# Performance work log

Hardware: AMD Instinct MI355X
Metric: run time of the kernel (lower is better)

Reference implementation:

```python
import jax, jax.numpy as jnp
import numpy as np

B, S, D = 2, 2048, 1024
N_QK, N_V, N_KNOW = 4096, 4096, 8192
N_HEADS = 16
MAX_K_QK, MAX_K_V, MAX_K_KNOW = 32, 32, 64
LN_EPS = 1e-6


def _unit_norm(key, shape, scale=1.0):
    x = jax.random.normal(key, shape, jnp.float32)
    return x / (jnp.linalg.norm(x, axis=-1, keepdims=True) + 1e-8) * scale


def setup_inputs() -> dict:
    key = jax.random.key(0)
    ks = jax.random.split(key, 12)
    return {
        "x": jax.random.normal(ks[0], (B, S, D), jnp.float32),
        "qk_emb": _unit_norm(ks[1], (N_QK, D)),
        "qk_w": _unit_norm(ks[2], (N_QK, D)),
        "v_emb": _unit_norm(ks[3], (N_V, D)),
        "v_w": _unit_norm(ks[4], (N_V, D)),
        "know_emb": _unit_norm(ks[5], (N_KNOW, D)),
        "know_w": _unit_norm(ks[6], (N_KNOW, D)),
        "tau_attn_k": jax.random.normal(ks[7], (D, 3), jnp.float32) * (1.0 / np.sqrt(D)),
        "tau_attn_b": jnp.zeros((3,), jnp.float32),
        "tau_know_k": jax.random.normal(ks[8], (D, 1), jnp.float32) * (1.0 / np.sqrt(D)),
        "tau_know_b": jnp.zeros((1,), jnp.float32),
        "expand_O": jax.random.normal(ks[9], (D, D), jnp.float32) * 0.02,
        "ln1_scale": jnp.ones((D,), jnp.float32),
        "ln1_bias": jnp.zeros((D,), jnp.float32),
        "ln2_scale": jnp.ones((D,), jnp.float32),
        "ln2_bias": jnp.zeros((D,), jnp.float32),
    }


def _layer_norm(x, scale, bias):
    mean = jnp.mean(x, axis=-1, keepdims=True)
    var = jnp.mean(jnp.square(x - mean), axis=-1, keepdims=True)
    return (x - mean) / jnp.sqrt(var + LN_EPS) * scale + bias


def threshold_gate(scores, tau, max_k):
    # scores: [B,S,N], tau: [B,S,1]
    raw = scores - tau
    gate = jnp.where(raw > 0, raw, 1e-8 * jnp.exp(raw))
    exp_gate = jnp.exp(gate) - 1.0
    topk_vals, _ = jax.lax.top_k(exp_gate, min(max_k, scores.shape[-1]))
    thr = topk_vals[:, :, -1:]
    exp_gate = jnp.where(exp_gate >= thr, exp_gate, 0.0)
    gate_sum = exp_gate.sum(axis=-1, keepdims=True) + 1e-8
    strength = jnp.tanh(exp_gate.max(axis=-1, keepdims=True))
    return exp_gate / gate_sum * strength


@jax.checkpoint
def sense_emit_full(x, emb, w, gate):
    # [B,S,D] @ [D,N] -> gated [B,S,N] -> [B,S,D]
    return ((x @ emb.T) * gate) @ w


def _block(x, qk_emb, qk_w, v_emb, v_w, know_emb, know_w,
           tau_attn_k, tau_attn_b, tau_know_k, tau_know_b,
           expand_O, ln1_scale, ln1_bias, ln2_scale, ln2_bias):
    # ---- attention circuit (deterministic; dropout = identity) ----
    normed = _layer_norm(x, ln1_scale, ln1_bias)
    scores_qk = normed @ qk_emb.T           # [B,S,N_QK]
    scores_v = normed @ v_emb.T             # [B,S,N_V]
    tau_all = normed @ tau_attn_k + tau_attn_b  # [B,S,3]
    g_Q = threshold_gate(scores_qk, tau_all[:, :, 0:1], MAX_K_QK)
    g_K = threshold_gate(scores_qk, tau_all[:, :, 1:2], MAX_K_QK)
    g_V = threshold_gate(scores_v, tau_all[:, :, 2:3], MAX_K_V)
    t_qk = 1.0 / qk_emb.shape[0]
    t_v = 1.0 / v_emb.shape[0]
    a_aux = (((g_Q.mean(axis=(0, 1)) - t_qk) ** 2).sum() * g_Q.shape[-1]
             + ((g_K.mean(axis=(0, 1)) - t_qk) ** 2).sum() * g_K.shape[-1]
             + ((g_V.mean(axis=(0, 1)) - t_v) ** 2).sum() * g_V.shape[-1])

    Q = sense_emit_full(normed, qk_emb, qk_w, g_Q)
    K = sense_emit_full(normed, qk_emb, qk_w, g_K)
    V = sense_emit_full(normed, v_emb, v_w, g_V)

    Bs, Ss, Ds = x.shape
    d_head = Ds // N_HEADS
    Q = Q.reshape(Bs, Ss, N_HEADS, d_head).transpose(0, 2, 1, 3)
    K = K.reshape(Bs, Ss, N_HEADS, d_head).transpose(0, 2, 1, 3)
    V = V.reshape(Bs, Ss, N_HEADS, d_head).transpose(0, 2, 1, 3)
    scale = jnp.sqrt(jnp.float32(d_head))
    attn = jnp.einsum('bhsd,bhtd->bhst', Q, K) / scale
    causal = jnp.tril(jnp.ones((Ss, Ss), dtype=jnp.bool_))
    attn = jnp.where(causal, attn, jnp.finfo(attn.dtype).min)
    attn = jax.nn.softmax(attn, axis=-1)
    out = jnp.einsum('bhst,bhtd->bhsd', attn, V)
    out = out.transpose(0, 2, 1, 3).reshape(Bs, Ss, Ds)
    out = out @ expand_O
    x = x + out

    # ---- knowledge circuit ----
    normed = _layer_norm(x, ln2_scale, ln2_bias)
    scores_k = normed @ know_emb.T          # [B,S,N_KNOW]
    tau_k = normed @ tau_know_k + tau_know_b
    gate = threshold_gate(scores_k, tau_k, MAX_K_KNOW)
    t_k = 1.0 / know_emb.shape[0]
    k_aux = ((gate.mean(axis=(0, 1)) - t_k) ** 2).sum() * know_emb.shape[0]
    know_out = sense_emit_full(normed, know_emb, know_w, gate)
    x = x + know_out
    return x, a_aux + k_aux


def reference(x, qk_emb, qk_w, v_emb, v_w, know_emb, know_w,
              tau_attn_k, tau_attn_b, tau_know_k, tau_know_b,
              expand_O, ln1_scale, ln1_bias, ln2_scale, ln2_bias):
    return _block(x, qk_emb, qk_w, v_emb, v_w, know_emb, know_w,
                  tau_attn_k, tau_attn_b, tau_know_k, tau_know_b,
                  expand_O, ln1_scale, ln1_bias, ln2_scale, ln2_bias)
```

## Files before the change

kernel.cpp:

```cpp
#include <hip/hip_runtime.h>

#define TOK   4096
#define DIM   1024
#define NQK   4096
#define NV    4096
#define NKN   8192
#define SLEN  2048
#define NH    16
#define DH    64
#define CAPA  48
#define CAPK  96
#define APAD  72

typedef float  f32x4  __attribute__((ext_vector_type(4)));
typedef short  short8 __attribute__((ext_vector_type(8)));
typedef unsigned int  u32;
typedef unsigned short u16;

__device__ __forceinline__ u16 f2bf(float f) {
    u32 u = __float_as_uint(f);
    u32 r = (u + 0x7fffu + ((u >> 16) & 1u)) >> 16;
    return (u16)r;
}
__device__ __forceinline__ float bf2f(u16 v) { return __uint_as_float(((u32)v) << 16); }

__device__ __forceinline__ u16 bfkey(u16 b) {
    return (b & 0x8000u) ? (u16)(~b) : (u16)(b | 0x8000u);
}
__device__ __forceinline__ u16 keybf(u16 k) {
    return (k & 0x8000u) ? (u16)(k & 0x7fffu) : (u16)(~k);
}

__device__ __forceinline__ f32x4 mfma_bf16(short8 a, short8 b, f32x4 c) {
    asm volatile("v_mfma_f32_16x16x32_bf16 %0, %1, %2, %0"
                 : "+v"(c) : "v"(a), "v"(b));
    return c;
}

__device__ __forceinline__ void gload16(const u16* g, u16* s) {
    __builtin_amdgcn_global_load_lds((const __attribute__((address_space(1))) void*)g,
                                     (__attribute__((address_space(3))) void*)s, 16, 0, 0);
}

__device__ __forceinline__ float blockReduceF(float v, float* red, int wave, int lane) {
#pragma unroll
    for (int off = 32; off > 0; off >>= 1) v += __shfl_xor(v, off);
    __syncthreads();
    if (lane == 0) red[wave] = v;
    __syncthreads();
    return red[0] + red[1] + red[2] + red[3];
}

__global__ __launch_bounds__(256) void k_convert_all(const float* __restrict__ p0,
                                                     const float* __restrict__ p1,
                                                     const float* __restrict__ p2,
                                                     const float* __restrict__ p3,
                                                     const float* __restrict__ p4,
                                                     const float* __restrict__ p5,
                                                     u16* __restrict__ o0, u16* __restrict__ o1,
                                                     u16* __restrict__ o2, u16* __restrict__ o3,
                                                     u16* __restrict__ o4, u16* __restrict__ o5) {
    const int S0 = 1048576, S1 = 2097152, S2 = 4194304, S3 = 5242880, S4 = 6291456, S5 = 8388608;
    for (int i = blockIdx.x * 256 + threadIdx.x; i < S5; i += gridDim.x * 256) {
        const float* in; u16* out; int off;
        if (i < S0)      { in = p0; out = o0; off = i; }
        else if (i < S1) { in = p1; out = o1; off = i - S0; }
        else if (i < S2) { in = p2; out = o2; off = i - S1; }
        else if (i < S3) { in = p3; out = o3; off = i - S2; }
        else if (i < S4) { in = p4; out = o4; off = i - S3; }
        else             { in = p5; out = o5; off = i - S4; }
        float4 v = reinterpret_cast<const float4*>(in)[off];
        reinterpret_cast<ushort4*>(out)[off] = make_ushort4(f2bf(v.x), f2bf(v.y), f2bf(v.z), f2bf(v.w));
    }
}

__global__ __launch_bounds__(256) void k_transpose_bf16(const float* __restrict__ in,
                                                        u16* __restrict__ out) {
    __shared__ float tile[32][33];
    int bx = blockIdx.x * 32;
    int by = blockIdx.y * 32;
    int tx = threadIdx.x & 31;
    int ty = threadIdx.x >> 5;
    for (int r = ty; r < 32; r += 8)
        tile[r][tx] = in[(size_t)(by + r) * DIM + bx + tx];
    __syncthreads();
    for (int r = ty; r < 32; r += 8)
        out[(size_t)(bx + r) * DIM + by + tx] = f2bf(tile[tx][r]);
}

__global__ __launch_bounds__(256) void k_ln_tau(const float* __restrict__ x,
                                                const float* __restrict__ sc,
                                                const float* __restrict__ bi,
                                                const float* __restrict__ tauk,
                                                const float* __restrict__ taub,
                                                int ntau,
                                                u16* __restrict__ nrm,
                                                float* __restrict__ tau_out) {
    __shared__ float red[4];
    int t = blockIdx.x, tid = threadIdx.x, wave = tid >> 6, lane = tid & 63;
    const float4 xv = reinterpret_cast<const float4*>(x + (size_t)t * DIM)[tid];
    float s = xv.x + xv.y + xv.z + xv.w;
    s = blockReduceF(s, red, wave, lane);
    float mean = s * (1.0f / DIM);
    float d0 = xv.x - mean, d1 = xv.y - mean, d2 = xv.z - mean, d3 = xv.w - mean;
    float ss = d0 * d0 + d1 * d1 + d2 * d2 + d3 * d3;
    ss = blockReduceF(ss, red, wave, lane);
    float rstd = rsqrtf(ss * (1.0f / DIM) + 1e-6f);
    const float4 scv = reinterpret_cast<const float4*>(sc)[tid];
    const float4 biv = reinterpret_cast<const float4*>(bi)[tid];
    float n0 = d0 * rstd * scv.x + biv.x;
    float n1 = d1 * rstd * scv.y + biv.y;
    float n2 = d2 * rstd * scv.z + biv.z;
    float n3 = d3 * rstd * scv.w + biv.w;
    ushort4 o = make_ushort4(f2bf(n0), f2bf(n1), f2bf(n2), f2bf(n3));
    reinterpret_cast<ushort4*>(nrm + (size_t)t * DIM)[tid] = o;
    int d = tid * 4;
    for (int j = 0; j < ntau; j++) {
        float p = n0 * tauk[(size_t)(d + 0) * ntau + j] + n1 * tauk[(size_t)(d + 1) * ntau + j]
                + n2 * tauk[(size_t)(d + 2) * ntau + j] + n3 * tauk[(size_t)(d + 3) * ntau + j];
        p = blockReduceF(p, red, wave, lane);
        if (tid == 0) tau_out[(size_t)t * ntau + j] = p + taub[j];
    }
}

template<int TAG, int KEYOUT>
__global__ __launch_bounds__(256) void k_gemm_bt(const u16* __restrict__ A,
                                                 const u16* __restrict__ B,
                                                 void* __restrict__ Cv,
                                                 int M, int N, int K,
                                                 const float* __restrict__ res) {
    __shared__ __align__(16) u16 As[4096];
    __shared__ __align__(16) u16 Bs[4096];
    int tid = threadIdx.x;
    int wave = tid >> 6, lane = tid & 63;
    int m0 = blockIdx.y * 128, n0 = blockIdx.x * 128;
    int wm = (wave >> 1) * 64, wn = (wave & 1) * 64;
    int kg = lane >> 4, l15 = lane & 15;

    const u16* gA0 = A + (size_t)(m0 + lane) * K + wave * 8;
    const u16* gA1 = A + (size_t)(m0 + 64 + lane) * K + wave * 8;
    const u16* gB0 = B + (size_t)(n0 + lane) * K + wave * 8;
    const u16* gB1 = B + (size_t)(n0 + 64 + lane) * K + wave * 8;
    u16* sA0 = As + wave * 1024;
    u16* sA1 = As + wave * 1024 + 512;
    u16* sB0 = Bs + wave * 1024;
    u16* sB1 = Bs + wave * 1024 + 512;

    f32x4 acc[4][4];
#pragma unroll
    for (int i = 0; i < 4; i++)
#pragma unroll
        for (int j = 0; j < 4; j++) { f32x4 z = {0.f, 0.f, 0.f, 0.f}; acc[i][j] = z; }

    for (int k0 = 0; k0 < K; k0 += 32) {
        __syncthreads();
        gload16(gA0 + k0, sA0);
        gload16(gA1 + k0, sA1);
        gload16(gB0 + k0, sB0);
        gload16(gB1 + k0, sB1);
        __syncthreads();
        short8 af[4], bg[4];
#pragma unroll
        for (int mi = 0; mi < 4; mi++) {
            int row = wm + mi * 16 + l15;
            af[mi] = *reinterpret_cast<const short8*>(&As[(kg * 128 + row) * 8]);
        }
#pragma unroll
        for (int ni = 0; ni < 4; ni++) {
            int row = wn + ni * 16 + l15;
            bg[ni] = *reinterpret_cast<const short8*>(&Bs[(kg * 128 + row) * 8]);
        }
#pragma unroll
        for (int mi = 0; mi < 4; mi++)
#pragma unroll
            for (int ni = 0; ni < 4; ni++)
                acc[mi][ni] = mfma_bf16(af[mi], bg[ni], acc[mi][ni]);
    }
    asm volatile("s_nop 7\n\ts_nop 7");
#pragma unroll
    for (int mi = 0; mi < 4; mi++) {
#pragma unroll
        for (int ni = 0; ni < 4; ni++) {
            int col = n0 + wn + ni * 16 + l15;
#pragma unroll
            for (int r = 0; r < 4; r++) {
                int rowm = m0 + wm + mi * 16 + (lane >> 4) * 4 + r;
                size_t idx = (size_t)rowm * N + col;
                float v = acc[mi][ni][r];
                if (KEYOUT) {
                    ((u16*)Cv)[idx] = bfkey(f2bf(v));
                } else {
                    if (res) v += res[idx];
                    ((float*)Cv)[idx] = v;
                }
            }
        }
    }
}

__global__ __launch_bounds__(256) void k_gate(const u16* __restrict__ keys_g, int NC, int ksel,
                                              int row_off,
                                              const float* __restrict__ tau, int tau_stride, int tcol0,
                                              int two,
                                              int* __restrict__ sel,
                                              float* __restrict__ vA, float* __restrict__ vB,
                                              int* __restrict__ cnt,
                                              float* __restrict__ csA, float* __restrict__ csB,
                                              int cap) {
    extern __shared__ u16 keys[];
    __shared__ int   hist[256];
    __shared__ int   scnt;
    __shared__ int   dsel;
    __shared__ int   knext;
    __shared__ int   sidx[CAPK];
    __shared__ float sraw[CAPK];
    int r = blockIdx.x, tid = threadIdx.x, wave = tid >> 6, lane = tid & 63;
    int t = row_off + r;

    const uint4* srow8 = reinterpret_cast<const uint4*>(keys_g + (size_t)r * NC);
    for (int c = tid; c < NC / 8; c += 256)
        reinterpret_cast<uint4*>(keys)[c] = srow8[c];
    if (tid == 0) scnt = 0;

    u32 prefix = 0;
    int krem = ksel;
#pragma unroll
    for (int pass = 0; pass < 2; pass++) {
        int shift = 8 - pass * 8;
        hist[tid] = 0;
        __syncthreads();
        u32 pmask = (pass == 0) ? 0u : 0xFF00u;
        for (int i = tid; i < NC; i += 256) {
            u32 ky = keys[i];
            if ((ky & pmask) == prefix)
                atomicAdd(&hist[(ky >> shift) & 255], 1);
        }
        __syncthreads();
        int v = hist[tid];
#pragma unroll
        for (int off = 1; off < 256; off <<= 1) {
            int other = (tid + off < 256) ? hist[tid + off] : 0;
            __syncthreads();
            v += other;
            hist[tid] = v;
            __syncthreads();
        }
        int sfx = v;
        int sfx_next = (tid < 255) ? hist[tid + 1] : 0;
        if (sfx >= krem && (tid == 255 || sfx_next < krem)) {
            dsel = tid;
            knext = krem - sfx_next;
        }
        __syncthreads();
        prefix |= ((u32)dsel) << shift;
        krem = knext;
        __syncthreads();
    }
    u32 thr = prefix;

    for (int i = tid; i < NC; i += 256) {
        u32 ky = keys[i];
        if (ky >= thr) {
            int p = atomicAdd(&scnt, 1);
            if (p < cap) {
                sidx[p] = i;
                sraw[p] = bf2f(keybf((u16)ky));
            }
        }
    }
    __syncthreads();
    int n = scnt < cap ? scnt : cap;
    if (tid == 0) cnt[t] = n;
    if (wave != 0) return;

    float tA = tau[(size_t)t * tau_stride + tcol0];
    float tB = two ? tau[(size_t)t * tau_stride + tcol0 + 1] : 0.f;
    float sumA = 0.f, mxA = -1e30f, sumB = 0.f, mxB = -1e30f;
    for (int i = lane; i < n; i += 64) {
        float sv = sraw[i];
        float rA = sv - tA;
        float gA = rA > 0.f ? rA : 1e-8f * expf(rA);
        float eA = expf(gA) - 1.0f;
        sumA += eA; mxA = fmaxf(mxA, eA);
        if (two) {
            float rB = sv - tB;
            float gB = rB > 0.f ? rB : 1e-8f * expf(rB);
            float eB = expf(gB) - 1.0f;
            sumB += eB; mxB = fmaxf(mxB, eB);
        }
    }
#pragma unroll
    for (int off = 32; off > 0; off >>= 1) {
        sumA += __shfl_xor(sumA, off); mxA = fmaxf(mxA, __shfl_xor(mxA, off));
        sumB += __shfl_xor(sumB, off); mxB = fmaxf(mxB, __shfl_xor(mxB, off));
    }
    float fA = tanhf(mxA) / (sumA + 1e-8f);
    float fB = tanhf(mxB) / (sumB + 1e-8f);
    for (int i = lane; i < n; i += 64) {
        float sv = sraw[i]; int ci = sidx[i];
        float rA = sv - tA;
        float gA = rA > 0.f ? rA : 1e-8f * expf(rA);
        float ga = (expf(gA) - 1.0f) * fA;
        sel[(size_t)t * cap + i] = ci;
        vA[(size_t)t * cap + i] = ga * sv;
        atomicAdd(&csA[ci], ga);
        if (two) {
            float rB = sv - tB;
            float gB = rB > 0.f ? rB : 1e-8f * expf(rB);
            float gb = (expf(gB) - 1.0f) * fB;
            vB[(size_t)t * cap + i] = gb * sv;
            atomicAdd(&csB[ci], gb);
        }
    }
}

__global__ __launch_bounds__(256) void k_gather2(const u16* __restrict__ w,
                                                 const int* __restrict__ sel,
                                                 const float* __restrict__ vA,
                                                 const float* __restrict__ vB,
                                                 const int* __restrict__ cnt, int cap,
                                                 u16* __restrict__ OA, u16* __restrict__ OB) {
    __shared__ int   sI[CAPK];
    __shared__ float sA[CAPK];
    __shared__ float sB[CAPK];
    int t = blockIdx.x, tid = threadIdx.x;
    int n = cnt[t];
    if (tid < n) { sI[tid] = sel[(size_t)t * cap + tid]; sA[tid] = vA[(size_t)t * cap + tid]; sB[tid] = vB[(size_t)t * cap + tid]; }
    __syncthreads();
    float a0 = 0, a1 = 0, a2 = 0, a3 = 0, b0 = 0, b1 = 0, b2 = 0, b3 = 0;
    for (int s = 0; s < n; s++) {
        const ushort4 wv = reinterpret_cast<const ushort4*>(w + (size_t)sI[s] * DIM)[tid];
        float w0 = bf2f(wv.x), w1 = bf2f(wv.y), w2 = bf2f(wv.z), w3 = bf2f(wv.w);
        float va = sA[s], vb = sB[s];
        a0 += va * w0; a1 += va * w1; a2 += va * w2; a3 += va * w3;
        b0 += vb * w0; b1 += vb * w1; b2 += vb * w2; b3 += vb * w3;
    }
    reinterpret_cast<ushort4*>(OA + (size_t)t * DIM)[tid] = make_ushort4(f2bf(a0), f2bf(a1), f2bf(a2), f2bf(a3));
    reinterpret_cast<ushort4*>(OB + (size_t)t * DIM)[tid] = make_ushort4(f2bf(b0), f2bf(b1), f2bf(b2), f2bf(b3));
}

__global__ __launch_bounds__(256) void k_gather1(const u16* __restrict__ w,
                                                 const int* __restrict__ sel,
                                                 const float* __restrict__ vv,
                                                 const int* __restrict__ cnt, int cap,
                                                 u16* __restrict__ O) {
    __shared__ int   sI[CAPK];
    __shared__ float sV[CAPK];
    int t = blockIdx.x, tid = threadIdx.x;
    int n = cnt[t];
    if (tid < n) { sI[tid] = sel[(size_t)t * cap + tid]; sV[tid] = vv[(size_t)t * cap + tid]; }
    __syncthreads();
    float a0 = 0, a1 = 0, a2 = 0, a3 = 0;
    for (int s = 0; s < n; s++) {
        const ushort4 wv = reinterpret_cast<const ushort4*>(w + (size_t)sI[s] * DIM)[tid];
        float va = sV[s];
        a0 += va * bf2f(wv.x); a1 += va * bf2f(wv.y); a2 += va * bf2f(wv.z); a3 += va * bf2f(wv.w);
    }
    reinterpret_cast<ushort4*>(O + (size_t)t * DIM)[tid] = make_ushort4(f2bf(a0), f2bf(a1), f2bf(a2), f2bf(a3));
}

__global__ __launch_bounds__(256) void k_gather_final(const u16* __restrict__ w,
                                                      const int* __restrict__ sel,
                                                      const float* __restrict__ vv,
                                                      const int* __restrict__ cnt, int cap,
                                                      float* __restrict__ io) {
    __shared__ int   sI[CAPK];
    __shared__ float sV[CAPK];
    int t = blockIdx.x, tid = threadIdx.x;
    int n = cnt[t];
    if (tid < n) { sI[tid] = sel[(size_t)t * cap + tid]; sV[tid] = vv[(size_t)t * cap + tid]; }
    __syncthreads();
    float4 base = reinterpret_cast<const float4*>(io + (size_t)t * DIM)[tid];
    float a0 = base.x, a1 = base.y, a2 = base.z, a3 = base.w;
    for (int s = 0; s < n; s++) {
        const ushort4 wv = reinterpret_cast<const ushort4*>(w + (size_t)sI[s] * DIM)[tid];
        float va = sV[s];
        a0 += va * bf2f(wv.x); a1 += va * bf2f(wv.y); a2 += va * bf2f(wv.z); a3 += va * bf2f(wv.w);
    }
    reinterpret_cast<float4*>(io + (size_t)t * DIM)[tid] = make_float4(a0, a1, a2, a3);
}

__global__ __launch_bounds__(256) void k_attn(const u16* __restrict__ Q,
                                              const u16* __restrict__ K,
                                              const u16* __restrict__ V,
                                              u16* __restrict__ O) {
    __shared__ __align__(16) u16 Qs[64 * APAD];
    __shared__ __align__(16) u16 Ks[64 * APAD];
    __shared__ __align__(16) u16 Vt[64 * APAD];
    __shared__ __align__(16) u16 Ps[4][16 * APAD];
    int tid = threadIdx.x, wave = tid >> 6, lane = tid & 63;
    int qt = gridDim.x - 1 - blockIdx.x;
    int h = blockIdx.y, bb = blockIdx.z;
    int q0 = qt * 64;
    size_t base = ((size_t)bb * SLEN) * DIM + (size_t)h * DH;
    int sr = tid >> 2, sc = (tid & 3) * 16;
    int g = lane >> 4, l15 = lane & 15;

    {
        const u16* qp = Q + base + (size_t)(q0 + sr) * DIM + sc;
        *reinterpret_cast<short8*>(&Qs[sr * APAD + sc])     = *reinterpret_cast<const short8*>(qp);
        *reinterpret_cast<short8*>(&Qs[sr * APAD + sc + 8]) = *reinterpret_cast<const short8*>(qp + 8);
    }
    __syncthreads();
    short8 qa0 = *reinterpret_cast<const short8*>(&Qs[(wave * 16 + l15) * APAD + g * 8]);
    short8 qa1 = *reinterpret_cast<const short8*>(&Qs[(wave * 16 + l15) * APAD + 32 + g * 8]);

    float m[4], l[4];
    f32x4 oacc[4];
#pragma unroll
    for (int i = 0; i < 4; i++) {
        m[i] = -1e30f; l[i] = 0.f;
        f32x4 z = {0.f, 0.f, 0.f, 0.f}; oacc[i] = z;
    }
    u16* pw = &Ps[wave][0];

    for (int kc = 0; kc <= qt; kc++) {
        __syncthreads();
        {
            const u16* kp = K + base + (size_t)(kc * 64 + sr) * DIM + sc;
            *reinterpret_cast<short8*>(&Ks[sr * APAD + sc])     = *reinterpret_cast<const short8*>(kp);
            *reinterpret_cast<short8*>(&Ks[sr * APAD + sc + 8]) = *reinterpret_cast<const short8*>(kp + 8);
            const u16* vp = V + base + (size_t)(kc * 64 + sr) * DIM + sc;
            short8 w0 = *reinterpret_cast<const short8*>(vp);
            short8 w1 = *reinterpret_cast<const short8*>(vp + 8);
            const u16* w0p = reinterpret_cast<const u16*>(&w0);
            const u16* w1p = reinterpret_cast<const u16*>(&w1);
#pragma unroll
            for (int j = 0; j < 16; j++) {
                int d = sc + j;
                int phys = (((sr >> 3) + d + (d >> 4)) & 7);
                Vt[d * APAD + phys * 8 + (sr & 7)] = (j < 8) ? w0p[j] : w1p[j - 8];
            }
        }
        __syncthreads();

        f32x4 s4[4];
#pragma unroll
        for (int ks = 0; ks < 4; ks++) {
            f32x4 z = {0.f, 0.f, 0.f, 0.f}; s4[ks] = z;
            short8 kb0 = *reinterpret_cast<const short8*>(&Ks[(ks * 16 + l15) * APAD + g * 8]);
            short8 kb1 = *reinterpret_cast<const short8*>(&Ks[(ks * 16 + l15) * APAD + 32 + g * 8]);
            s4[ks] = mfma_bf16(qa0, kb0, s4[ks]);
            s4[ks] = mfma_bf16(qa1, kb1, s4[ks]);
        }
        asm volatile("s_nop 7\n\ts_nop 7");

        int key_base = kc * 64 + l15;
#pragma unroll
        for (int ks = 0; ks < 4; ks++) {
            int key = key_base + ks * 16;
#pragma unroll
            for (int r = 0; r < 4; r++) {
                int q_abs = q0 + wave * 16 + g * 4 + r;
                float sv = s4[ks][r] * 0.125f;
                s4[ks][r] = (key > q_abs) ? -1e30f : sv;
            }
        }

#pragma unroll
        for (int r = 0; r < 4; r++) {
            float mx = fmaxf(fmaxf(s4[0][r], s4[1][r]), fmaxf(s4[2][r], s4[3][r]));
            mx = fmaxf(mx, __shfl_xor(mx, 1));
            mx = fmaxf(mx, __shfl_xor(mx, 2));
            mx = fmaxf(mx, __shfl_xor(mx, 4));
            mx = fmaxf(mx, __shfl_xor(mx, 8));
            float mnew = fmaxf(m[r], mx);
            float al = __expf(m[r] - mnew);
            m[r] = mnew;
            float p0 = __expf(s4[0][r] - mnew);
            float p1 = __expf(s4[1][r] - mnew);
            float p2 = __expf(s4[2][r] - mnew);
            float p3 = __expf(s4[3][r] - mnew);
            float ps = p0 + p1 + p2 + p3;
            ps += __shfl_xor(ps, 1);
            ps += __shfl_xor(ps, 2);
            ps += __shfl_xor(ps, 4);
            ps += __shfl_xor(ps, 8);
            l[r] = l[r] * al + ps;
#pragma unroll
            for (int ds_ = 0; ds_ < 4; ds_++) oacc[ds_][r] *= al;
            int row = g * 4 + r;
            pw[row * APAD +  0 + l15] = f2bf(p0);
            pw[row * APAD + 16 + l15] = f2bf(p1);
            pw[row * APAD + 32 + l15] = f2bf(p2);
            pw[row * APAD + 48 + l15] = f2bf(p3);
        }

        short8 pa0 = *reinterpret_cast<const short8*>(&pw[l15 * APAD + g * 8]);
        short8 pa1 = *reinterpret_cast<const short8*>(&pw[l15 * APAD + 32 + g * 8]);
#pragma unroll
        for (int dsub = 0; dsub < 4; dsub++) {
            int d = dsub * 16 + l15;
            int rot = d + (d >> 4);
            short8 vb0 = *reinterpret_cast<const short8*>(&Vt[d * APAD + (((0 + g) + rot) & 7) * 8]);
            short8 vb1 = *reinterpret_cast<const short8*>(&Vt[d * APAD + (((4 + g) + rot) & 7) * 8]);
            oacc[dsub] = mfma_bf16(pa0, vb0, oacc[dsub]);
            oacc[dsub] = mfma_bf16(pa1, vb1, oacc[dsub]);
        }
    }
    asm volatile("s_nop 7\n\ts_nop 7");

#pragma unroll
    for (int r = 0; r < 4; r++) {
        float inv = 1.0f / l[r];
        int row = q0 + wave * 16 + g * 4 + r;
#pragma unroll
        for (int dsub = 0; dsub < 4; dsub++) {
            O[base + (size_t)row * DIM + dsub * 16 + l15] = f2bf(oacc[dsub][r] * inv);
        }
    }
}

__global__ __launch_bounds__(256) void k_aux(const float* __restrict__ cs,
                                             float* __restrict__ out_aux) {
    __shared__ float red[4];
    int gtid = blockIdx.x * 256 + threadIdx.x;
    float acc = 0.f;
    for (int i = gtid; i < 3 * 4096 + 8192; i += gridDim.x * 256) {
        float mean = cs[i] * (1.0f / 4096.0f);
        float tN, Nf;
        if (i < 12288) { tN = 1.0f / 4096.0f; Nf = 4096.0f; }
        else           { tN = 1.0f / 8192.0f; Nf = 8192.0f; }
        float d = mean - tN;
        acc += d * d * Nf;
    }
    acc = blockReduceF(acc, red, threadIdx.x >> 6, threadIdx.x & 63);
    if (threadIdx.x == 0) atomicAdd(out_aux, acc);
}

extern "C" void kernel_launch(void* const* d_in, const int* in_sizes, int n_in,
                              void* d_out, int out_size, void* d_ws, size_t ws_size,
                              hipStream_t stream) {
    const float* x         = (const float*)d_in[0];
    const float* qk_emb    = (const float*)d_in[1];
    const float* qk_w      = (const float*)d_in[2];
    const float* v_emb     = (const float*)d_in[3];
    const float* v_w       = (const float*)d_in[4];
    const float* know_emb  = (const float*)d_in[5];
    const float* know_w    = (const float*)d_in[6];
    const float* tau_attn_k = (const float*)d_in[7];
    const float* tau_attn_b = (const float*)d_in[8];
    const float* tau_know_k = (const float*)d_in[9];
    const float* tau_know_b = (const float*)d_in[10];
    const float* expand_O  = (const float*)d_in[11];
    const float* ln1_s     = (const float*)d_in[12];
    const float* ln1_b     = (const float*)d_in[13];
    const float* ln2_s     = (const float*)d_in[14];
    const float* ln2_b     = (const float*)d_in[15];
    float* out = (float*)d_out;
    char*  ws  = (char*)d_ws;

    u16*   nrm_bf   = (u16*)(ws + 0);
    u16*   qkemb_bf = (u16*)(ws + 8388608);
    u16*   vemb_bf  = (u16*)(ws + 16777216);
    u16*   knemb_bf = (u16*)(ws + 25165824);
    u16*   expT_bf  = (u16*)(ws + 41943040);
    u16*   attn_bf  = (u16*)(ws + 44040192);
    u16*   qkw_bf   = (u16*)(ws + 52428800);
    u16*   vw_bf    = (u16*)(ws + 60817408);
    u16*   knw_bf   = (u16*)(ws + 69206016);
    u16*   Qb       = (u16*)(ws + 85983232);
    u16*   Kb       = (u16*)(ws + 94371840);
    u16*   Vb       = (u16*)(ws + 102760448);
    u16*   keysbuf  = (u16*)(ws + 111149056);
    int*   selQK    = (int*)(ws + 178257920);
    float* valQ     = (float*)(ws + 179044352);
    float* valK     = (float*)(ws + 179830784);
    int*   selV     = (int*)(ws + 180617216);
    float* valV     = (float*)(ws + 181403648);
    int*   selKn    = (int*)(ws + 182190080);
    float* valKn    = (float*)(ws + 183762944);
    int*   cntQK    = (int*)(ws + 185335808);
    int*   cntV     = (int*)(ws + 185352192);
    int*   cntKn    = (int*)(ws + 185368576);
    float* tauA     = (float*)(ws + 185384960);
    float* tauKn    = (float*)(ws + 185434112);
    float* colsum   = (float*)(ws + 185450496);
    const size_t WS_NEEDED = 185532416;
    if (ws_size < WS_NEEDED) return;

    float* colQ = colsum, *colK = colsum + 4096, *colV = colsum + 8192, *colKn = colsum + 12288;

    hipMemsetAsync(colsum, 0, 20480 * sizeof(float), stream);
    hipMemsetAsync(out + (size_t)TOK * DIM, 0, sizeof(float), stream);

    k_convert_all<<<2048, 256, 0, stream>>>(qk_emb, v_emb, know_emb, qk_w, v_w, know_w,
                                            qkemb_bf, vemb_bf, knemb_bf, qkw_bf, vw_bf, knw_bf);
    k_transpose_bf16<<<dim3(32, 32), 256, 0, stream>>>(expand_O, expT_bf);

    k_ln_tau<<<TOK, 256, 0, stream>>>(x, ln1_s, ln1_b, tau_attn_k, tau_attn_b, 3, nrm_bf, tauA);

    k_gemm_bt<0, 1><<<dim3(NQK / 128, TOK / 128), 256, 0, stream>>>(nrm_bf, qkemb_bf, keysbuf, TOK, NQK, DIM, nullptr);
    k_gate<<<TOK, 256, NQK * sizeof(u16), stream>>>(keysbuf, NQK, 32, 0, tauA, 3, 0, 1,
                                                    selQK, valQ, valK, cntQK, colQ, colK, CAPA);
    k_gemm_bt<1, 1><<<dim3(NV / 128, TOK / 128), 256, 0, stream>>>(nrm_bf, vemb_bf, keysbuf, TOK, NV, DIM, nullptr);
    k_gate<<<TOK, 256, NV * sizeof(u16), stream>>>(keysbuf, NV, 32, 0, tauA, 3, 2, 0,
                                                   selV, valV, nullptr, cntV, colV, nullptr, CAPA);

    k_gather2<<<TOK, 256, 0, stream>>>(qkw_bf, selQK, valQ, valK, cntQK, CAPA, Qb, Kb);
    k_gather1<<<TOK, 256, 0, stream>>>(vw_bf, selV, valV, cntV, CAPA, Vb);

    k_attn<<<dim3(SLEN / 64, NH, 2), 256, 0, stream>>>(Qb, Kb, Vb, attn_bf);

    k_gemm_bt<2, 0><<<dim3(DIM / 128, TOK / 128), 256, 0, stream>>>(attn_bf, expT_bf, out, TOK, DIM, DIM, x);

    k_ln_tau<<<TOK, 256, 0, stream>>>(out, ln2_s, ln2_b, tau_know_k, tau_know_b, 1, nrm_bf, tauKn);

    for (int c = 0; c < 2; c++) {
        k_gemm_bt<3, 1><<<dim3(NKN / 128, 2048 / 128), 256, 0, stream>>>(
            nrm_bf + (size_t)c * 2048 * DIM, knemb_bf, keysbuf, 2048, NKN, DIM, nullptr);
        k_gate<<<2048, 256, NKN * sizeof(u16), stream>>>(keysbuf, NKN, 64, c * 2048, tauKn, 1, 0, 0,
                                                         selKn, valKn, nullptr, cntKn, colKn, nullptr, CAPK);
    }

    k_gather_final<<<TOK, 256, 0, stream>>>(knw_bf, selKn, valKn, cntKn, CAPK, out);

    k_aux<<<20, 256, 0, stream>>>(colsum, out + (size_t)TOK * DIM);
}
```

Before: 818.6 us.

## Fuse gating with sparse weight gather and reorder attention grid

Merges the threshold-gate kernel with the following sparse gather/emit kernels. Each block selects its top-k indices, computes gate values in shared memory, then immediately accumulates the selected weight rows, with the gather loop unrolled by four. This removes the global sel/val/cnt round trip and three kernel launches. The attention grid is also reordered so heads and batches vary fastest with the query tile outermost, which changes the causal load-balancing order. The cost is that gating now holds the large keys buffer in shared memory through the gather phase, which may lower occupancy.

```diff
diff --git a/kernel.cpp b/kernel.cpp
--- a/kernel.cpp
+++ b/kernel.cpp
@@ -198,24 +198,25 @@
     }
 }
 
-__global__ __launch_bounds__(256) void k_gate(const u16* __restrict__ keys_g, int NC, int ksel,
-                                              int row_off,
-                                              const float* __restrict__ tau, int tau_stride, int tcol0,
-                                              int two,
-                                              int* __restrict__ sel,
-                                              float* __restrict__ vA, float* __restrict__ vB,
-                                              int* __restrict__ cnt,
-                                              float* __restrict__ csA, float* __restrict__ csB,
-                                              int cap) {
+template<int TWO, int RES>
+__global__ __launch_bounds__(256) void k_gate_emit(const u16* __restrict__ keys_g, int NC, int ksel,
+                                                   int row_off,
+                                                   const float* __restrict__ tau, int tau_stride, int tcol0,
+                                                   const u16* __restrict__ w,
+                                                   u16* __restrict__ OA, u16* __restrict__ OB,
+                                                   float* __restrict__ io,
+                                                   float* __restrict__ csA, float* __restrict__ csB) {
     extern __shared__ u16 keys[];
     __shared__ int   hist[256];
     __shared__ int   scnt;
     __shared__ int   dsel;
     __shared__ int   knext;
     __shared__ int   sidx[CAPK];
-    __shared__ float sraw[CAPK];
+    __shared__ float svA[CAPK];
+    __shared__ float svB[CAPK];
     int r = blockIdx.x, tid = threadIdx.x, wave = tid >> 6, lane = tid & 63;
     int t = row_off + r;
+    const int cap = TWO ? CAPA : (RES ? CAPK : CAPA);
 
     const uint4* srow8 = reinterpret_cast<const uint4*>(keys_g + (size_t)r * NC);
     for (int c = tid; c < NC / 8; c += 256)
@@ -264,120 +265,111 @@
             int p = atomicAdd(&scnt, 1);
             if (p < cap) {
                 sidx[p] = i;
-                sraw[p] = bf2f(keybf((u16)ky));
+                svA[p] = bf2f(keybf((u16)ky));
             }
         }
     }
     __syncthreads();
     int n = scnt < cap ? scnt : cap;
-    if (tid == 0) cnt[t] = n;
-    if (wave != 0) return;
-
-    float tA = tau[(size_t)t * tau_stride + tcol0];
-    float tB = two ? tau[(size_t)t * tau_stride + tcol0 + 1] : 0.f;
-    float sumA = 0.f, mxA = -1e30f, sumB = 0.f, mxB = -1e30f;
-    for (int i = lane; i < n; i += 64) {
-        float sv = sraw[i];
-        float rA = sv - tA;
-        float gA = rA > 0.f ? rA : 1e-8f * expf(rA);
-        float eA = expf(gA) - 1.0f;
-        sumA += eA; mxA = fmaxf(mxA, eA);
-        if (two) {
-            float rB = sv - tB;
-            float gB = rB > 0.f ? rB : 1e-8f * expf(rB);
-            float eB = expf(gB) - 1.0f;
-            sumB += eB; mxB = fmaxf(mxB, eB);
-        }
-    }
-#pragma unroll
-    for (int off = 32; off > 0; off >>= 1) {
-        sumA += __shfl_xor(sumA, off); mxA = fmaxf(mxA, __shfl_xor(mxA, off));
-        sumB += __shfl_xor(sumB, off); mxB = fmaxf(mxB, __shfl_xor(mxB, off));
-    }
-    float fA = tanhf(mxA) / (sumA + 1e-8f);
-    float fB = tanhf(mxB) / (sumB + 1e-8f);
-    for (int i = lane; i < n; i += 64) {
-        float sv = sraw[i]; int ci = sidx[i];
-        float rA = sv - tA;
-        float gA = rA > 0.f ? rA : 1e-8f * expf(rA);
-        float ga = (expf(gA) - 1.0f) * fA;
-        sel[(size_t)t * cap + i] = ci;
-        vA[(size_t)t * cap + i] = ga * sv;
-        atomicAdd(&csA[ci], ga);
-        if (two) {
-            float rB = sv - tB;
-            float gB = rB > 0.f ? rB : 1e-8f * expf(rB);
-            float gb = (expf(gB) - 1.0f) * fB;
-            vB[(size_t)t * cap + i] = gb * sv;
-            atomicAdd(&csB[ci], gb);
-        }
-    }
-}
-
-__global__ __launch_bounds__(256) void k_gather2(const u16* __restrict__ w,
-                                                 const int* __restrict__ sel,
-                                                 const float* __restrict__ vA,
-                                                 const float* __restrict__ vB,
-                                                 const int* __restrict__ cnt, int cap,
-                                                 u16* __restrict__ OA, u16* __restrict__ OB) {
-    __shared__ int   sI[CAPK];
-    __shared__ float sA[CAPK];
-    __shared__ float sB[CAPK];
-    int t = blockIdx.x, tid = threadIdx.x;
-    int n = cnt[t];
-    if (tid < n) { sI[tid] = sel[(size_t)t * cap + tid]; sA[tid] = vA[(size_t)t * cap + tid]; sB[tid] = vB[(size_t)t * cap + tid]; }
+
+    if (wave == 0) {
+        float tA = tau[(size_t)t * tau_stride + tcol0];
+        float tB = TWO ? tau[(size_t)t * tau_stride + tcol0 + 1] : 0.f;
+        float sumA = 0.f, mxA = -1e30f, sumB = 0.f, mxB = -1e30f;
+        float sv0 = (lane < n) ? svA[lane] : 0.f;
+        float sv1 = (lane + 64 < n) ? svA[lane + 64] : 0.f;
+        for (int i = lane; i < n; i += 64) {
+            float sv = svA[i];
+            float rA = sv - tA;
+            float gA = rA > 0.f ? rA : 1e-8f * expf(rA);
+            float eA = expf(gA) - 1.0f;
+            sumA += eA; mxA = fmaxf(mxA, eA);
+            if (TWO) {
+                float rB = sv - tB;
+                float gB = rB > 0.f ? rB : 1e-8f * expf(rB);
+                float eB = expf(gB) - 1.0f;
+                sumB += eB; mxB = fmaxf(mxB, eB);
+            }
+        }
+#pragma unroll
+        for (int off = 32; off > 0; off >>= 1) {
+            sumA += __shfl_xor(sumA, off); mxA = fmaxf(mxA, __shfl_xor(mxA, off));
+            sumB += __shfl_xor(sumB, off); mxB = fmaxf(mxB, __shfl_xor(mxB, off));
+        }
+        float fA = tanhf(mxA) / (sumA + 1e-8f);
+        float fB = tanhf(mxB) / (sumB + 1e-8f);
+        if (lane < n) {
+            float sv = sv0; int ci = sidx[lane];
+            float rA = sv - tA;
+            float gA = rA > 0.f ? rA : 1e-8f * expf(rA);
+            float ga = (expf(gA) - 1.0f) * fA;
+            svA[lane] = ga * sv;
+            atomicAdd(&csA[ci], ga);
+            if (TWO) {
+                float rB = sv - tB;
+                float gB = rB > 0.f ? rB : 1e-8f * expf(rB);
+                float gb = (expf(gB) - 1.0f) * fB;
+                svB[lane] = gb * sv;
+                atomicAdd(&csB[ci], gb);
+            }
+        }
+        if (lane + 64 < n) {
+            float sv = sv1; int ci = sidx[lane + 64];
+            float rA = sv - tA;
+            float gA = rA > 0.f ? rA : 1e-8f * expf(rA);
+            float ga = (expf(gA) - 1.0f) * fA;
+            svA[lane + 64] = ga * sv;
+            atomicAdd(&csA[ci], ga);
+            if (TWO) {
+                float rB = sv - tB;
+                float gB = rB > 0.f ? rB : 1e-8f * expf(rB);
+                float gb = (expf(gB) - 1.0f) * fB;
+                svB[lane + 64] = gb * sv;
+                atomicAdd(&csB[ci], gb);
+            }
+        }
+    }
     __syncthreads();
+
     float a0 = 0, a1 = 0, a2 = 0, a3 = 0, b0 = 0, b1 = 0, b2 = 0, b3 = 0;
-    for (int s = 0; s < n; s++) {
-        const ushort4 wv = reinterpret_cast<const ushort4*>(w + (size_t)sI[s] * DIM)[tid];
-        float w0 = bf2f(wv.x), w1 = bf2f(wv.y), w2 = bf2f(wv.z), w3 = bf2f(wv.w);
-        float va = sA[s], vb = sB[s];
-        a0 += va * w0; a1 += va * w1; a2 += va * w2; a3 += va * w3;
-        b0 += vb * w0; b1 += vb * w1; b2 += vb * w2; b3 += vb * w3;
-    }
-    reinterpret_cast<ushort4*>(OA + (size_t)t * DIM)[tid] = make_ushort4(f2bf(a0), f2bf(a1), f2bf(a2), f2bf(a3));
-    reinterpret_cast<ushort4*>(OB + (size_t)t * DIM)[tid] = make_ushort4(f2bf(b0), f2bf(b1), f2bf(b2), f2bf(b3));
-}
-
-__global__ __launch_bounds__(256) void k_gather1(const u16* __restrict__ w,
-                                                 const int* __restrict__ sel,
-                                                 const float* __restrict__ vv,
-                                                 const int* __restrict__ cnt, int cap,
-                                                 u16* __restrict__ O) {
-    __shared__ int   sI[CAPK];
-    __shared__ float sV[CAPK];
-    int t = blockIdx.x, tid = threadIdx.x;
-    int n = cnt[t];
-    if (tid < n) { sI[tid] = sel[(size_t)t * cap + tid]; sV[tid] = vv[(size_t)t * cap + tid]; }
-    __syncthreads();
-    float a0 = 0, a1 = 0, a2 = 0, a3 = 0;
-    for (int s = 0; s < n; s++) {
-        const ushort4 wv = reinterpret_cast<const ushort4*>(w + (size_t)sI[s] * DIM)[tid];
-        float va = sV[s];
+    float4 base;
+    if (RES) base = reinterpret_cast<const float4*>(io + (size_t)t * DIM)[tid];
+    int s = 0;
+    for (; s + 4 <= n; s += 4) {
+        const ushort4 w0 = reinterpret_cast<const ushort4*>(w + (size_t)sidx[s]     * DIM)[tid];
+        const ushort4 w1 = reinterpret_cast<const ushort4*>(w + (size_t)sidx[s + 1] * DIM)[tid];
+        const ushort4 w2 = reinterpret_cast<const ushort4*>(w + (size_t)sidx[s + 2] * DIM)[tid];
+        const ushort4 w3 = reinterpret_cast<const ushort4*>(w + (size_t)sidx[s + 3] * DIM)[tid];
+        float vA0 = svA[s], vA1 = svA[s + 1], vA2 = svA[s + 2], vA3 = svA[s + 3];
+        a0 += vA0 * bf2f(w0.x) + vA1 * bf2f(w1.x) + vA2 * bf2f(w2.x) + vA3 * bf2f(w3.x);
+        a1 += vA0 * bf2f(w0.y) + vA1 * bf2f(w1.y) + vA2 * bf2f(w2.y) + vA3 * bf2f(w3.y);
+        a2 += vA0 * bf2f(w0.z) + vA1 * bf2f(w1.z) + vA2 * bf2f(w2.z) + vA3 * bf2f(w3.z);
+        a3 += vA0 * bf2f(w0.w) + vA1 * bf2f(w1.w) + vA2 * bf2f(w2.w) + vA3 * bf2f(w3.w);
+        if (TWO) {
+            float vB0 = svB[s], vB1 = svB[s + 1], vB2 = svB[s + 2], vB3 = svB[s + 3];
+            b0 += vB0 * bf2f(w0.x) + vB1 * bf2f(w1.x) + vB2 * bf2f(w2.x) + vB3 * bf2f(w3.x);
+            b1 += vB0 * bf2f(w0.y) + vB1 * bf2f(w1.y) + vB2 * bf2f(w2.y) + vB3 * bf2f(w3.y);
+            b2 += vB0 * bf2f(w0.z) + vB1 * bf2f(w1.z) + vB2 * bf2f(w2.z) + vB3 * bf2f(w3.z);
+            b3 += vB0 * bf2f(w0.w) + vB1 * bf2f(w1.w) + vB2 * bf2f(w2.w) + vB3 * bf2f(w3.w);
+        }
+    }
+    for (; s < n; s++) {
+        const ushort4 wv = reinterpret_cast<const ushort4*>(w + (size_t)sidx[s] * DIM)[tid];
+        float va = svA[s];
         a0 += va * bf2f(wv.x); a1 += va * bf2f(wv.y); a2 += va * bf2f(wv.z); a3 += va * bf2f(wv.w);
-    }
-    reinterpret_cast<ushort4*>(O + (size_t)t * DIM)[tid] = make_ushort4(f2bf(a0), f2bf(a1), f2bf(a2), f2bf(a3));
-}
-
-__global__ __launch_bounds__(256) void k_gather_final(const u16* __restrict__ w,
-                                                      const int* __restrict__ sel,
-                                                      const float* __restrict__ vv,
-                                                      const int* __restrict__ cnt, int cap,
-                                                      float* __restrict__ io) {
-    __shared__ int   sI[CAPK];
-    __shared__ float sV[CAPK];
-    int t = blockIdx.x, tid = threadIdx.x;
-    int n = cnt[t];
-    if (tid < n) { sI[tid] = sel[(size_t)t * cap + tid]; sV[tid] = vv[(size_t)t * cap + tid]; }
-    __syncthreads();
-    float4 base = reinterpret_cast<const float4*>(io + (size_t)t * DIM)[tid];
-    float a0 = base.x, a1 = base.y, a2 = base.z, a3 = base.w;
-    for (int s = 0; s < n; s++) {
-        const ushort4 wv = reinterpret_cast<const ushort4*>(w + (size_t)sI[s] * DIM)[tid];
-        float va = sV[s];
-        a0 += va * bf2f(wv.x); a1 += va * bf2f(wv.y); a2 += va * bf2f(wv.z); a3 += va * bf2f(wv.w);
-    }
-    reinterpret_cast<float4*>(io + (size_t)t * DIM)[tid] = make_float4(a0, a1, a2, a3);
+        if (TWO) {
+            float vb = svB[s];
+            b0 += vb * bf2f(wv.x); b1 += vb * bf2f(wv.y); b2 += vb * bf2f(wv.z); b3 += vb * bf2f(wv.w);
+        }
+    }
+    if (RES) {
+        reinterpret_cast<float4*>(io + (size_t)t * DIM)[tid] =
+            make_float4(base.x + a0, base.y + a1, base.z + a2, base.w + a3);
+    } else {
+        reinterpret_cast<ushort4*>(OA + (size_t)t * DIM)[tid] = make_ushort4(f2bf(a0), f2bf(a1), f2bf(a2), f2bf(a3));
+        if (TWO)
+            reinterpret_cast<ushort4*>(OB + (size_t)t * DIM)[tid] = make_ushort4(f2bf(b0), f2bf(b1), f2bf(b2), f2bf(b3));
+    }
 }
 
 __global__ __launch_bounds__(256) void k_attn(const u16* __restrict__ Q,
@@ -389,8 +381,7 @@
     __shared__ __align__(16) u16 Vt[64 * APAD];
     __shared__ __align__(16) u16 Ps[4][16 * APAD];
     int tid = threadIdx.x, wave = tid >> 6, lane = tid & 63;
-    int qt = gridDim.x - 1 - blockIdx.x;
-    int h = blockIdx.y, bb = blockIdx.z;
+    int h = blockIdx.x, bb = blockIdx.y, qt = blockIdx.z;
     int q0 = qt * 64;
     size_t base = ((size_t)bb * SLEN) * DIM + (size_t)h * DH;
     int sr = tid >> 2, sc = (tid & 3) * 16;
@@ -563,16 +554,6 @@
     u16*   Kb       = (u16*)(ws + 94371840);
     u16*   Vb       = (u16*)(ws + 102760448);
     u16*   keysbuf  = (u16*)(ws + 111149056);
-    int*   selQK    = (int*)(ws + 178257920);
-    float* valQ     = (float*)(ws + 179044352);
-    float* valK     = (float*)(ws + 179830784);
-    int*   selV     = (int*)(ws + 180617216);
-    float* valV     = (float*)(ws + 181403648);
-    int*   selKn    = (int*)(ws + 182190080);
-    float* valKn    = (float*)(ws + 183762944);
-    int*   cntQK    = (int*)(ws + 185335808);
-    int*   cntV     = (int*)(ws + 185352192);
-    int*   cntKn    = (int*)(ws + 185368576);
     float* tauA     = (float*)(ws + 185384960);
     float* tauKn    = (float*)(ws + 185434112);
     float* colsum   = (float*)(ws + 185450496);
@@ -591,16 +572,13 @@
     k_ln_tau<<<TOK, 256, 0, stream>>>(x, ln1_s, ln1_b, tau_attn_k, tau_attn_b, 3, nrm_bf, tauA);
 
     k_gemm_bt<0, 1><<<dim3(NQK / 128, TOK / 128), 256, 0, stream>>>(nrm_bf, qkemb_bf, keysbuf, TOK, NQK, DIM, nullptr);
-    k_gate<<<TOK, 256, NQK * sizeof(u16), stream>>>(keysbuf, NQK, 32, 0, tauA, 3, 0, 1,
-                                                    selQK, valQ, valK, cntQK, colQ, colK, CAPA);
+    k_gate_emit<1, 0><<<TOK, 256, NQK * sizeof(u16), stream>>>(keysbuf, NQK, 32, 0, tauA, 3, 0,
+                                                               qkw_bf, Qb, Kb, nullptr, colQ, colK);
     k_gemm_bt<1, 1><<<dim3(NV / 128, TOK / 128), 256, 0, stream>>>(nrm_bf, vemb_bf, keysbuf, TOK, NV, DIM, nullptr);
-    k_gate<<<TOK, 256, NV * sizeof(u16), stream>>>(keysbuf, NV, 32, 0, tauA, 3, 2, 0,
-                                                   selV, valV, nullptr, cntV, colV, nullptr, CAPA);
-
-    k_gather2<<<TOK, 256, 0, stream>>>(qkw_bf, selQK, valQ, valK, cntQK, CAPA, Qb, Kb);
-    k_gather1<<<TOK, 256, 0, stream>>>(vw_bf, selV, valV, cntV, CAPA, Vb);
-
-    k_attn<<<dim3(SLEN / 64, NH, 2), 256, 0, stream>>>(Qb, Kb, Vb, attn_bf);
+    k_gate_emit<0, 0><<<TOK, 256, NV * sizeof(u16), stream>>>(keysbuf, NV, 32, 0, tauA, 3, 2,
+                                                              vw_bf, Vb, nullptr, nullptr, colV, nullptr);
+
+    k_attn<<<dim3(NH, 2, SLEN / 64), 256, 0, stream>>>(Qb, Kb, Vb, attn_bf);
 
     k_gemm_bt<2, 0><<<dim3(DIM / 128, TOK / 128), 256, 0, stream>>>(attn_bf, expT_bf, out, TOK, DIM, DIM, x);
 
@@ -609,11 +587,9 @@
     for (int c = 0; c < 2; c++) {
         k_gemm_bt<3, 1><<<dim3(NKN / 128, 2048 / 128), 256, 0, stream>>>(
             nrm_bf + (size_t)c * 2048 * DIM, knemb_bf, keysbuf, 2048, NKN, DIM, nullptr);
-        k_gate<<<2048, 256, NKN * sizeof(u16), stream>>>(keysbuf, NKN, 64, c * 2048, tauKn, 1, 0, 0,
-                                                         selKn, valKn, nullptr, cntKn, colKn, nullptr, CAPK);
-    }
-
-    k_gather_final<<<TOK, 256, 0, stream>>>(knw_bf, selKn, valKn, cntKn, CAPK, out);
+        k_gate_emit<0, 1><<<2048, 256, NKN * sizeof(u16), stream>>>(keysbuf, NKN, 64, c * 2048, tauKn, 1, 0,
+                                                                    knw_bf, nullptr, nullptr, out, colKn, nullptr);
+    }
 
     k_aux<<<20, 256, 0, stream>>>(colsum, out + (size_t)TOK * DIM);
 }
```

Result: faster. 743.9 us (-9.1%).
